# Kernel tuning notes

Hardware: AMD Instinct MI355X
Metric: run time of the kernel (lower is better)

Reference implementation:

```python
import jax, jax.numpy as jnp
import numpy as np

B, HH, WW, C, HEADS = 2, 128, 128, 256, 8
D = C // HEADS


def setup_inputs() -> dict:
    key = jax.random.key(0)
    ks = jax.random.split(key, 24)
    def nrm(k, shape, s=0.02):
        return jax.random.normal(k, shape, jnp.float32) * s
    inp = {
        'x_2': jax.random.normal(ks[0], (B, HH, WW, C), jnp.float32),
        'x_4': jax.random.normal(ks[1], (B, HH, WW, C), jnp.float32),
        'x_8': jax.random.normal(ks[2], (B, HH, WW, C), jnp.float32),
        'y':   jax.random.normal(ks[3], (B, HH, WW, C), jnp.float32),
        'Wqm': nrm(ks[4], (C, C)), 'Wkm': nrm(ks[5], (C, C)), 'Wvm': nrm(ks[6], (C, C)),
        'Wk2': nrm(ks[7], (C, C)), 'Wv2': nrm(ks[8], (C, C)),
        'Wk4': nrm(ks[9], (C, C)), 'Wv4': nrm(ks[10], (C, C)),
        'Wk8': nrm(ks[11], (C, C)), 'Wv8': nrm(ks[12], (C, C)),
        'rescalem': jnp.ones((HEADS, 1, 1), jnp.float32),
        'rescale2': jnp.ones((HEADS, 1, 1), jnp.float32),
        'rescale4': jnp.ones((HEADS, 1, 1), jnp.float32),
        'rescale8': jnp.ones((HEADS, 1, 1), jnp.float32),
        'Wproj': nrm(ks[13], (C, C)), 'bproj': jnp.zeros((C,), jnp.float32),
        'Wpos1': nrm(ks[14], (C, 1, 3, 3)), 'Wpos2': nrm(ks[15], (C, 1, 3, 3)),
    }
    return inp


def _l2norm(x):
    # F.normalize(p=2, dim=-1): x / max(||x||_2, eps)
    return x / jnp.maximum(jnp.linalg.norm(x, axis=-1, keepdims=True), 1e-12)


def _heads_T(t):
    # (b, n, h*d) -> (b, h, d, n)  (split heads then transpose last two dims)
    b, n, _ = t.shape
    return t.reshape(b, n, HEADS, D).transpose(0, 2, 3, 1)


def _dwconv(x, w):
    # x: NCHW, w: (C,1,3,3) depthwise
    return jax.lax.conv_general_dilated(
        x, w, (1, 1), 'SAME',
        dimension_numbers=('NCHW', 'OIHW', 'NCHW'),
        feature_group_count=C)


def reference(x_2, x_4, x_8, y,
              Wqm, Wkm, Wvm, Wk2, Wv2, Wk4, Wv4, Wk8, Wv8,
              rescalem, rescale2, rescale4, rescale8,
              Wproj, bproj, Wpos1, Wpos2):
    b, h, w, c = y.shape
    n = h * w
    x2 = x_2.reshape(b, n, c)
    x4 = x_4.reshape(b, n, c)
    x8 = x_8.reshape(b, n, c)
    yf = y.reshape(b, n, c)

    q_inpm = yf @ Wqm.T
    v_inpm = yf @ Wvm.T
    qm = _l2norm(_heads_T(q_inpm))  # (b,heads,d,n), L2-normalized over n

    def branch(k_inp, v_inp, rescale):
        k = _l2norm(_heads_T(k_inp))   # (b,heads,d,n)
        v = _heads_T(v_inp)            # (b,heads,d,n)
        attn = jnp.einsum('bhdn,bhen->bhde', k, qm) * rescale  # (b,heads,d,d)
        attn = jax.nn.softmax(attn, axis=-1)
        return jnp.einsum('bhde,bhen->bhdn', attn, v)

    # NOTE: original code uses rescale4 for the x8 branch (faithful to source).
    xo = (branch(yf @ Wkm.T, v_inpm, rescalem)
          + branch(x2 @ Wk2.T, x2 @ Wv2.T, rescale2)
          + branch(x4 @ Wk4.T, x4 @ Wv4.T, rescale4)
          + branch(x8 @ Wk8.T, x8 @ Wv8.T, rescale4))

    # (b,heads,d,n) -> (b,n,heads*d)
    xo = xo.transpose(0, 3, 1, 2).reshape(b, n, HEADS * D)
    out_c = (xo @ Wproj.T + bproj).reshape(b, h, w, c)

    p = v_inpm.reshape(b, h, w, c).transpose(0, 3, 1, 2)  # NCHW
    p = _dwconv(p, Wpos1)
    p = jax.nn.gelu(p, approximate=False)
    p = _dwconv(p, Wpos2)
    out_p = p.transpose(0, 2, 3, 1)

    return out_c + out_p
```

## Files before the change

kernel.cpp:

```cpp
#include <hip/hip_runtime.h>
#include <hip/hip_bf16.h>
#include <math.h>

typedef short bf16x8 __attribute__((ext_vector_type(8)));
typedef float f32x4 __attribute__((ext_vector_type(4)));

#define MFMA16(a,b,c) __builtin_amdgcn_mfma_f32_16x16x32_bf16(a,b,c,0,0,0)

__device__ inline short f2bf(float f){
  union{ __hip_bfloat16 h; short s; } u;
  u.h = __float2bfloat16(f);
  return u.s;
}
__device__ inline float bf2f(short s){
  uint32_t u = ((uint32_t)(uint16_t)s) << 16;
  return __builtin_bit_cast(float, u);
}
__device__ inline void store8bf(short* dst, float4 a, float4 b){
  union{ short s[8]; int4 q; } u;
  u.s[0]=f2bf(a.x); u.s[1]=f2bf(a.y); u.s[2]=f2bf(a.z); u.s[3]=f2bf(a.w);
  u.s[4]=f2bf(b.x); u.s[5]=f2bf(b.y); u.s[6]=f2bf(b.z); u.s[7]=f2bf(b.w);
  *(int4*)dst = u.q;
}

__device__ inline void gld16(const void* g, void* l){
  __builtin_amdgcn_global_load_lds(
      (const __attribute__((address_space(1))) unsigned int*)g,
      (__attribute__((address_space(3))) unsigned int*)l, 16, 0, 0);
}

#define BARC() do{ asm volatile("":::"memory"); __builtin_amdgcn_s_barrier(); \
                   asm volatile("":::"memory"); }while(0)

__global__ __launch_bounds__(256) void k_cvt(const float* __restrict__ src, short* __restrict__ dst, int n){
  int i = blockIdx.x*256 + threadIdx.x;
  if(i < n) dst[i] = f2bf(src[i]);
}

__global__ __launch_bounds__(256) void k_cvtN(const float* __restrict__ src, short* __restrict__ dst,
                                              int n, int ncpy){
  int i = blockIdx.x*256 + threadIdx.x;
  if(i >= n) return;
  float s = src[i];
  for(int c=1;c<ncpy;++c) s += src[i + (size_t)c*917504];
  dst[i] = f2bf(s);
}

__global__ __launch_bounds__(256) void k_wvt(const float* __restrict__ wm, const float* __restrict__ w2,
                                             const float* __restrict__ w4, const float* __restrict__ w8,
                                             short* __restrict__ wvT){
  int t = blockIdx.x*256 + threadIdx.x;
  int br = t >> 16; int rem = t & 65535; int a = rem >> 8, j = rem & 255;
  const float* w = (br==0)? wm : (br==1)? w2 : (br==2)? w4 : w8;
  wvT[t] = f2bf(w[j*256 + a]);
}

__global__ __launch_bounds__(256) void k_wT(const float* __restrict__ w1, const float* __restrict__ w2,
                                            float* __restrict__ wT){
  int t = blockIdx.x*256 + threadIdx.x;
  if(t >= 4608) return;
  int cv = t / 2304; int rem = t % 2304; int tap = rem >> 8; int c = rem & 255;
  const float* w = cv ? w2 : w1;
  wT[t] = w[c*9 + tap];
}

__global__ __launch_bounds__(256) void k_prep(const float* __restrict__ Wvm, const float* __restrict__ Wv2,
                                              const float* __restrict__ Wv4, const float* __restrict__ Wv8,
                                              const float* __restrict__ Wp1, const float* __restrict__ Wp2,
                                              short* __restrict__ WvmB, short* __restrict__ wvT,
                                              float* __restrict__ wT){
  int bx = blockIdx.x, t = threadIdx.x;
  if(bx < 256){
    int i = bx*256 + t;
    WvmB[i] = f2bf(Wvm[i]);
  } else if(bx < 1280){
    int i = (bx-256)*256 + t;
    int br = i >> 16; int rem = i & 65535; int a = rem >> 8, j = rem & 255;
    const float* w = (br==0)? Wvm : (br==1)? Wv2 : (br==2)? Wv4 : Wv8;
    wvT[i] = f2bf(w[j*256 + a]);
  } else {
    int i = (bx-1280)*256 + t;
    if(i < 4608){
      int cv = i / 2304; int rem = i % 2304; int tap = rem >> 8; int c = rem & 255;
      const float* w = cv ? Wp2 : Wp1;
      wT[i] = w[c*9 + tap];
    }
  }
}

__device__ inline void at_write4(short* base, int row, int l, float4 v){
  union{ short s[4]; int2 q; } u;
  u.s[0]=f2bf(v.x); u.s[1]=f2bf(v.y); u.s[2]=f2bf(v.z); u.s[3]=f2bf(v.w);
  int byte = row*512 + 8*l;
  byte ^= ((row&7)<<4);
  *(int2*)((char*)base + byte) = u.q;
}
__device__ inline void at_write4c(short* base, int row, int c4, float4 v){
  union{ short s[4]; int2 q; } u;
  u.s[0]=f2bf(v.x); u.s[1]=f2bf(v.y); u.s[2]=f2bf(v.z); u.s[3]=f2bf(v.w);
  int byte = row*512 + c4*8;
  byte ^= ((row&7)<<4);
  *(int2*)((char*)base + byte) = u.q;
}
__device__ inline bf16x8 at_read8(const short* base, int row, int kk, int q){
  int byte = row*512 + kk*64 + q*16;
  byte ^= ((row&7)<<4);
  return *(const bf16x8*)((const char*)base + byte);
}

__global__ __launch_bounds__(256) void k_pack(const float* __restrict__ x2, const float* __restrict__ x4,
                                              const float* __restrict__ x8, const float* __restrict__ y,
                                              short* __restrict__ xt, int sb0){
  int sb = blockIdx.z + sb0; int s = sb >> 1, b = sb & 1;
  const float* src = ((s==0)? y : (s==1)? x2 : (s==2)? x4 : x8) + (size_t)b*16384*256;
  __shared__ int4 tile4[2048];
  char* tile = (char*)tile4;
  int t = threadIdx.x;
  int cg = t & 63, ng = t >> 6;
  int n0 = blockIdx.x*64;
  const float* p0 = src + (size_t)(n0 + ng*8)*256 + cg*4;
  const float* p1 = src + (size_t)(n0 + 32 + ng*8)*256 + cg*4;
  union{ float4 q; float f[4]; } v0[8], v1[8];
  #pragma unroll
  for(int r=0;r<8;++r) v0[r].q = *(const float4*)(p0 + (size_t)r*256);
  #pragma unroll
  for(int r=0;r<8;++r) v1[r].q = *(const float4*)(p1 + (size_t)r*256);
  #pragma unroll
  for(int i=0;i<4;++i){
    int c = cg*4 + i;
    int byte = c*64 + ((ng ^ ((c>>1)&3))<<4);
    byte ^= ((byte>>8)&7)<<4;
    union{ short s8[8]; int4 q; } u;
    #pragma unroll
    for(int r=0;r<8;++r) u.s8[r] = f2bf(v0[r].f[i]);
    *(int4*)(tile + byte) = u.q;
    #pragma unroll
    for(int r=0;r<8;++r) u.s8[r] = f2bf(v1[r].f[i]);
    *(int4*)(tile + 16384 + byte) = u.q;
  }
  __syncthreads();
  short* outb = xt + ((size_t)sb*512 + blockIdx.x*2)*8192;
  #pragma unroll
  for(int ti=0; ti<2; ++ti)
    #pragma unroll
    for(int j=0;j<4;++j){
      int addr = j*4096 + t*16;
      int sa = addr ^ (((addr>>8)&7)<<4);
      *(int4*)((char*)outb + ti*16384 + addr) = *(const int4*)(tile + ti*16384 + sa);
    }
}

__global__ __launch_bounds__(256) void k_packy(const float* __restrict__ y, const short* __restrict__ wB,
                                               short* __restrict__ xt, short* __restrict__ vm){
  int b = blockIdx.z;
  const float* src = y + (size_t)b*16384*256;
  __shared__ int4 tile4[2048];
  __shared__ short at[64*256];
  char* tile = (char*)tile4;
  int t = threadIdx.x;
  int cg = t & 63, ng = t >> 6;
  int n0 = blockIdx.x*64;
  const float* p0 = src + (size_t)(n0 + ng*8)*256 + cg*4;
  const float* p1 = src + (size_t)(n0 + 32 + ng*8)*256 + cg*4;
  union{ float4 q; float f[4]; } v0[8], v1[8];
  #pragma unroll
  for(int r=0;r<8;++r) v0[r].q = *(const float4*)(p0 + (size_t)r*256);
  #pragma unroll
  for(int r=0;r<8;++r) v1[r].q = *(const float4*)(p1 + (size_t)r*256);
  #pragma unroll
  for(int i=0;i<4;++i){
    int c = cg*4 + i;
    int byte = c*64 + ((ng ^ ((c>>1)&3))<<4);
    byte ^= ((byte>>8)&7)<<4;
    union{ short s8[8]; int4 q; } u;
    #pragma unroll
    for(int r=0;r<8;++r) u.s8[r] = f2bf(v0[r].f[i]);
    *(int4*)(tile + byte) = u.q;
    #pragma unroll
    for(int r=0;r<8;++r) u.s8[r] = f2bf(v1[r].f[i]);
    *(int4*)(tile + 16384 + byte) = u.q;
  }
  #pragma unroll
  for(int r=0;r<8;++r){
    at_write4c(at, ng*8 + r, cg, v0[r].q);
    at_write4c(at, 32 + ng*8 + r, cg, v1[r].q);
  }
  __syncthreads();
  short* outb = xt + ((size_t)b*512 + blockIdx.x*2)*8192;
  #pragma unroll
  for(int ti=0; ti<2; ++ti)
    #pragma unroll
    for(int j=0;j<4;++j){
      int addr = j*4096 + t*16;
      int sa = addr ^ (((addr>>8)&7)<<4);
      *(int4*)((char*)outb + ti*16384 + addr) = *(const int4*)(tile + ti*16384 + sa);
    }
  int l = t & 63, w = t >> 6;
  size_t m0 = (size_t)b*16384 + n0;
  f32x4 acc[4][4];
  #pragma unroll
  for(int i=0;i<4;++i)
    #pragma unroll
    for(int n2=0;n2<4;++n2) acc[i][n2] = (f32x4){0.f,0.f,0.f,0.f};
  #pragma unroll
  for(int kk=0; kk<8; ++kk){
    bf16x8 a[4];
    #pragma unroll
    for(int rt=0;rt<4;++rt) a[rt] = at_read8(at, rt*16 + (l&15), kk, l>>4);
    #pragma unroll
    for(int nt=0;nt<4;++nt){
      int bc = (w*4+nt)*16 + (l&15);
      bf16x8 bb = *(const bf16x8*)&wB[(size_t)bc*256 + kk*32 + 8*(l>>4)];
      #pragma unroll
      for(int rt=0;rt<4;++rt) acc[rt][nt] = MFMA16(a[rt], bb, acc[rt][nt]);
    }
  }
  #pragma unroll
  for(int rt=0;rt<4;++rt)
    #pragma unroll
    for(int nt=0;nt<4;++nt)
      #pragma unroll
      for(int r=0;r<4;++r){
        size_t row = m0 + rt*16 + 4*(l>>4) + r;
        int col = (w*4+nt)*16 + (l&15);
        vm[row*256 + col] = f2bf(acc[rt][nt][r]);
      }
}

__device__ inline bf16x8 tfrag(const short* base, int c, int hi){
  int byte = c*64 + ((hi ^ ((c>>1)&3))<<4);
  return *(const bf16x8*)((const char*)base + byte);
}

__global__ __launch_bounds__(512) void k_cov(const short* __restrict__ xt, float* __restrict__ covF,
                                             int plain){
  int jb = blockIdx.x;
  int ck = blockIdx.y;
  int j = jb >> 1, b = jb & 1;
  int t = threadIdx.x, l = t & 63, w = t >> 6;
  int lr = l & 15, hi = l >> 4;
  int wr = w >> 1, wc = w & 1;
  __shared__ short lds2[2][32768];
  int su = (j < 4) ? 0 : (j - 3);
  int sv = (j == 0) ? 0 : ((j < 4) ? j : (j - 3));
  int sym = (su == sv);
  const short* Ug = xt + (size_t)(su*2+b)*512*8192;
  const short* Vg = xt + (size_t)(sv*2+b)*512*8192;
  int nt0 = ck*32;

  f32x4 acc[4][8];
  #pragma unroll
  for(int i=0;i<4;++i)
    #pragma unroll
    for(int n2=0;n2<8;++n2) acc[i][n2] = (f32x4){0.f,0.f,0.f,0.f};

  #define STAGE_T_S(bufi, tt, kk) do{                                           \
    const short* Ut_ = Ug + (size_t)(nt0+(kk))*8192;                            \
    short* dst_ = &lds2[bufi][(tt)*16384];                                      \
    _Pragma("unroll")                                                           \
    for(int i_=0;i_<2;++i_){ int ch_ = w*2+i_;                                  \
      gld16(Ut_ + ch_*512 + l*8, dst_ + ch_*512); }                             \
  }while(0)
  #define STAGE_T_A(bufi, tt, kk) do{                                           \
    const short* Ut_ = Ug + (size_t)(nt0+(kk))*8192;                            \
    const short* Vt_ = Vg + (size_t)(nt0+(kk))*8192;                            \
    short* dst_ = &lds2[bufi][(tt)*16384];                                      \
    _Pragma("unroll")                                                           \
    for(int i_=0;i_<4;++i_){ int ch_ = w*4+i_;                                  \
      const short* g_ = (ch_<16) ? (Ut_ + ch_*512 + l*8)                        \
                                 : (Vt_ + (ch_-16)*512 + l*8);                  \
      gld16(g_, dst_ + ch_*512); }                                              \
  }while(0)
  #define COMPUTE_T(bufp, vofs) do{                                             \
    const short* Ub_ = bufp;                                                    \
    const short* Vb_ = Ub_ + (vofs);                                            \
    bf16x8 a_[4];                                                               \
    _Pragma("unroll")                                                           \
    for(int rt_=0;rt_<4;++rt_)                                                  \
      a_[rt_] = tfrag(Ub_, wr*64 + rt_*16 + lr, hi);                            \
    _Pragma("unroll")                                                           \
    for(int nt_=0;nt_<8;++nt_){                                                 \
      bf16x8 bb_ = tfrag(Vb_, wc*128 + nt_*16 + lr, hi);                        \
      _Pragma("unroll")                                                         \
      for(int rt_=0;rt_<4;++rt_)                                                \
        acc[rt_][nt_] = MFMA16(a_[rt_], bb_, acc[rt_][nt_]);                    \
    }                                                                           \
  }while(0)

  if(sym){
    STAGE_T_S(0,0,0); STAGE_T_S(0,1,1); STAGE_T_S(1,0,2); STAGE_T_S(1,1,3);
    asm volatile("s_waitcnt vmcnt(4)":::"memory");
    BARC();
    #pragma unroll 1
    for(int p=0;p<16;++p){
      const short* base = &lds2[p&1][0];
      COMPUTE_T(base, 0);
      COMPUTE_T(base + 16384, 0);
      if(p==15) break;
      BARC();
      if(p < 14){
        STAGE_T_S(p&1, 0, 2*p+4); STAGE_T_S(p&1, 1, 2*p+5);
        asm volatile("s_waitcnt vmcnt(4)":::"memory");
      } else {
        asm volatile("s_waitcnt vmcnt(0)":::"memory");
      }
      BARC();
    }
  } else {
    STAGE_T_A(0,0,0); STAGE_T_A(0,1,1); STAGE_T_A(1,0,2); STAGE_T_A(1,1,3);
    asm volatile("s_waitcnt vmcnt(8)":::"memory");
    BARC();
    #pragma unroll 1
    for(int p=0;p<16;++p){
      const short* base = &lds2[p&1][0];
      COMPUTE_T(base, 8192);
      COMPUTE_T(base + 16384, 8192);
      if(p==15) break;
      BARC();
      if(p < 14){
        STAGE_T_A(p&1, 0, 2*p+4); STAGE_T_A(p&1, 1, 2*p+5);
        asm volatile("s_waitcnt vmcnt(8)":::"memory");
      } else {
        asm volatile("s_waitcnt vmcnt(0)":::"memory");
      }
      BARC();
    }
  }
  #undef STAGE_T_S
  #undef STAGE_T_A
  #undef COMPUTE_T

  if(plain){
    float* cov = covF + (size_t)ck*917504 + (size_t)jb*65536;
    #pragma unroll
    for(int rt=0;rt<4;++rt)
      #pragma unroll
      for(int nt=0;nt<8;++nt)
        #pragma unroll
        for(int r=0;r<4;++r){
          int row = wr*64 + rt*16 + 4*hi + r;
          int col = wc*128 + nt*16 + lr;
          cov[(size_t)row*256 + col] = acc[rt][nt][r];
        }
  } else {
    float* cov = covF + (size_t)jb*65536;
    #pragma unroll
    for(int rt=0;rt<4;++rt)
      #pragma unroll
      for(int nt=0;nt<8;++nt)
        #pragma unroll
        for(int r=0;r<4;++r){
          int row = wr*64 + rt*16 + 4*hi + r;
          int col = wc*128 + nt*16 + lr;
          atomicAdd(&cov[(size_t)row*256 + col], acc[rt][nt][r]);
        }
  }
}

__device__ inline void mm_32x256(const short (*wA)[264], const short* __restrict__ covbf,
                                 short (*tmp)[264], int t){
  int l = t & 63, w = t >> 6;
  int mt = w >> 1, ntb = (w & 1)*8;
  f32x4 acc[8];
  #pragma unroll
  for(int i=0;i<8;++i) acc[i] = (f32x4){0.f,0.f,0.f,0.f};
  #pragma unroll
  for(int kk=0; kk<8; ++kk){
    bf16x8 a = *(const bf16x8*)&wA[16*mt + (l&15)][kk*32 + 8*(l>>4)];
    #pragma unroll
    for(int n=0; n<8; ++n){
      int j = (ntb+n)*16 + (l&15);
      bf16x8 bb = *(const bf16x8*)&covbf[(size_t)j*256 + kk*32 + 8*(l>>4)];
      acc[n] = MFMA16(a, bb, acc[n]);
    }
  }
  #pragma unroll
  for(int n=0;n<8;++n)
    #pragma unroll
    for(int r=0;r<4;++r)
      tmp[16*mt + 4*(l>>4) + r][(ntb+n)*16 + (l&15)] = f2bf(acc[n][r]);
}
__device__ inline void mm_32x32(const short (*A)[264], const short (*Bw)[264], float (*M)[33], int t){
  int l = t & 63, w = t >> 6;
  int mt = w >> 1, nt = w & 1;
  f32x4 acc = (f32x4){0.f,0.f,0.f,0.f};
  #pragma unroll
  for(int kk=0; kk<8; ++kk){
    bf16x8 a = *(const bf16x8*)&A[16*mt + (l&15)][kk*32 + 8*(l>>4)];
    bf16x8 b = *(const bf16x8*)&Bw[16*nt + (l&15)][kk*32 + 8*(l>>4)];
    acc = MFMA16(a, b, acc);
  }
  #pragma unroll
  for(int r=0;r<4;++r)
    M[16*mt + 4*(l>>4) + r][16*nt + (l&15)] = acc[r];
}

__global__ __launch_bounds__(256) void k_attn(
    const float* __restrict__ Wq, const float* __restrict__ Wkm, const float* __restrict__ Wk2,
    const float* __restrict__ Wk4, const float* __restrict__ Wk8,
    const float* __restrict__ rsm, const float* __restrict__ rs2, const float* __restrict__ rs4,
    const short* __restrict__ covB, float* __restrict__ Aout){
  int h = blockIdx.x, b = blockIdx.y, br = blockIdx.z;
  int t = threadIdx.x;
  __shared__ short wk[32][264], wq[32][264], tmp[32][264];
  __shared__ float Ml[32][33];
  __shared__ float nrm[64];
  const float* Wk = (br==0)? Wkm : (br==1)? Wk2 : (br==2)? Wk4 : Wk8;
  {
    int d = t >> 3, c0 = (t & 7)*32;
    const float* pk = Wk + (size_t)(h*32+d)*256 + c0;
    const float* pq = Wq + (size_t)(h*32+d)*256 + c0;
    #pragma unroll
    for(int i=0;i<32;i+=8){
      float4 a1 = *(const float4*)(pk+i), a2 = *(const float4*)(pk+i+4);
      store8bf(&wk[d][c0+i], a1, a2);
      float4 b1 = *(const float4*)(pq+i), b2 = *(const float4*)(pq+i+4);
      store8bf(&wq[d][c0+i], b1, b2);
    }
  }
  __syncthreads();
  const short* cxy = covB + (size_t)(br*2+b)*65536;
  const short* cxx = (br==0)? cxy : covB + (size_t)(8 + (br-1)*2 + b)*65536;
  const short* cyy = covB + (size_t)b*65536;
  mm_32x256(wk, cxx, tmp, t); __syncthreads();
  mm_32x32(tmp, wk, Ml, t);   __syncthreads();
  if(t < 32) nrm[t] = Ml[t][t];
  __syncthreads();
  mm_32x256(wq, cyy, tmp, t); __syncthreads();
  mm_32x32(tmp, wq, Ml, t);   __syncthreads();
  if(t < 32) nrm[32+t] = Ml[t][t];
  __syncthreads();
  mm_32x256(wk, cxy, tmp, t); __syncthreads();
  mm_32x32(tmp, wq, Ml, t);   __syncthreads();
  if(t < 32){
    int d = t;
    const float* rs = (br==0)? rsm : (br==1)? rs2 : rs4;
    float rsv = rs[h];
    float invk = 1.f / fmaxf(sqrtf(fmaxf(nrm[d], 0.f)), 1e-12f);
    float lg[32]; float mx = -1e30f;
    #pragma unroll
    for(int e=0;e<32;++e){
      float invq = 1.f / fmaxf(sqrtf(fmaxf(nrm[32+e], 0.f)), 1e-12f);
      float v = Ml[d][e] * invk * invq * rsv;
      lg[e] = v; mx = fmaxf(mx, v);
    }
    float sum = 0.f;
    #pragma unroll
    for(int e=0;e<32;++e){ lg[e] = expf(lg[e]-mx); sum += lg[e]; }
    float inv = 1.f/sum;
    float* Ao = Aout + ((size_t)((br*2+b)*8 + h))*1024 + d*32;
    #pragma unroll
    for(int e=0;e<32;++e) Ao[e] = lg[e]*inv;
  }
}

__global__ __launch_bounds__(256) void k_qfold(const float* __restrict__ Wproj, const float* __restrict__ Ain,
                                               const short* __restrict__ wvT, short* __restrict__ qf){
  int cg = blockIdx.x, b = blockIdx.y, br = blockIdx.z;
  int t = threadIdx.x;
  __shared__ float Al[8*1036];
  __shared__ short pl[32][264];
  const float* Ag = Ain + (size_t)((br*2+b)*8)*1024;
  for(int i=t; i<8192; i+=256){
    int hh = i >> 10, dd = (i >> 5) & 31, ee = i & 31;
    Al[hh*1036 + dd*32 + ee] = Ag[i];
  }
  __syncthreads();
  {
    int c = cg*32 + (t >> 3), h = t & 7;
    const float* wpr = Wproj + (size_t)c*256 + h*32;
    float wp[32];
    #pragma unroll
    for(int i=0;i<32;i+=4){
      float4 v = *(const float4*)(wpr+i);
      wp[i]=v.x; wp[i+1]=v.y; wp[i+2]=v.z; wp[i+3]=v.w;
    }
    float pv[32];
    #pragma unroll
    for(int e=0;e<32;++e) pv[e]=0.f;
    const float* Ah = Al + h*1036;
    #pragma unroll
    for(int d=0; d<32; ++d){
      float wpd = wp[d];
      #pragma unroll
      for(int e=0;e<32;e+=4){
        float4 av = *(const float4*)&Ah[d*32+e];
        pv[e]   += wpd*av.x; pv[e+1] += wpd*av.y;
        pv[e+2] += wpd*av.z; pv[e+3] += wpd*av.w;
      }
    }
    #pragma unroll
    for(int e=0;e<32;++e) pl[t>>3][h*32+e] = f2bf(pv[e]);
  }
  __syncthreads();
  {
    int l = t & 63, w = t >> 6, mt = w >> 1, ntb = (w & 1)*8;
    const short* wvt = wvT + (size_t)br*65536;
    f32x4 acc[8];
    #pragma unroll
    for(int i=0;i<8;++i) acc[i] = (f32x4){0.f,0.f,0.f,0.f};
    #pragma unroll
    for(int kk=0; kk<8; ++kk){
      bf16x8 a = *(const bf16x8*)&pl[16*mt + (l&15)][kk*32 + 8*(l>>4)];
      #pragma unroll
      for(int n=0;n<8;++n){
        int arow = (ntb+n)*16 + (l&15);
        bf16x8 bb = *(const bf16x8*)&wvt[(size_t)arow*256 + kk*32 + 8*(l>>4)];
        acc[n] = MFMA16(a, bb, acc[n]);
      }
    }
    short* qfp = qf + (size_t)(br*2+b)*65536;
    #pragma unroll
    for(int n=0;n<8;++n)
      #pragma unroll
      for(int r=0;r<4;++r){
        int row = cg*32 + 16*mt + 4*(l>>4) + r;
        int col = (ntb+n)*16 + (l&15);
        qfp[(size_t)row*256 + col] = f2bf(acc[n][r]);
      }
  }
}

__global__ __launch_bounds__(256,2) void k_vm(const float* __restrict__ y, const short* __restrict__ wB,
                                              short* __restrict__ vm){
  int t = threadIdx.x, l = t & 63, w = t >> 6;
  size_t m0 = (size_t)blockIdx.x*64;
  __shared__ short at[64*256];
  #pragma unroll
  for(int rr=0; rr<16; ++rr){
    int row = w*16 + rr;
    float4 v = *(const float4*)(y + (m0+row)*256 + 4*l);
    at_write4(at, row, l, v);
  }
  __syncthreads();
  f32x4 acc[4][4];
  #pragma unroll
  for(int i=0;i<4;++i)
    #pragma unroll
    for(int n2=0;n2<4;++n2) acc[i][n2] = (f32x4){0.f,0.f,0.f,0.f};
  #pragma unroll
  for(int kk=0; kk<8; ++kk){
    bf16x8 a[4];
    #pragma unroll
    for(int rt=0;rt<4;++rt) a[rt] = at_read8(at, rt*16 + (l&15), kk, l>>4);
    #pragma unroll
    for(int nt=0;nt<4;++nt){
      int bc = (w*4+nt)*16 + (l&15);
      bf16x8 bb = *(const bf16x8*)&wB[(size_t)bc*256 + kk*32 + 8*(l>>4)];
      #pragma unroll
      for(int rt=0;rt<4;++rt) acc[rt][nt] = MFMA16(a[rt], bb, acc[rt][nt]);
    }
  }
  #pragma unroll
  for(int rt=0;rt<4;++rt)
    #pragma unroll
    for(int nt=0;nt<4;++nt)
      #pragma unroll
      for(int r=0;r<4;++r){
        size_t row = m0 + rt*16 + 4*(l>>4) + r;
        int col = (w*4+nt)*16 + (l&15);
        vm[row*256 + col] = f2bf(acc[rt][nt][r]);
      }
}

__global__ __launch_bounds__(256) void k_conv(const short* __restrict__ in, const float* __restrict__ wT,
                                              short* __restrict__ out, int do_gelu){
  int tid = blockIdx.x*256 + threadIdx.x;
  int cg = tid & 31; int pix = tid >> 5;
  int x = pix & 127, yy = (pix >> 7) & 127, b = pix >> 14;
  int c0 = cg*8;
  float acc[8];
  #pragma unroll
  for(int i=0;i<8;++i) acc[i]=0.f;
  #pragma unroll
  for(int ky=0; ky<3; ++ky){
    int sy = yy + ky - 1;
    if(sy < 0 || sy > 127) continue;
    #pragma unroll
    for(int kx=0; kx<3; ++kx){
      int sx = x + kx - 1;
      if(sx < 0 || sx > 127) continue;
      const float* wp = wT + (ky*3+kx)*256 + c0;
      float4 w0 = *(const float4*)wp;
      float4 w1 = *(const float4*)(wp+4);
      const short* p = in + ((size_t)(((b<<7)+sy)<<7) + sx)*256 + c0;
      union{ int4 q; short s[8]; } u;
      u.q = *(const int4*)p;
      acc[0] += bf2f(u.s[0])*w0.x; acc[1] += bf2f(u.s[1])*w0.y;
      acc[2] += bf2f(u.s[2])*w0.z; acc[3] += bf2f(u.s[3])*w0.w;
      acc[4] += bf2f(u.s[4])*w1.x; acc[5] += bf2f(u.s[5])*w1.y;
      acc[6] += bf2f(u.s[6])*w1.z; acc[7] += bf2f(u.s[7])*w1.w;
    }
  }
  if(do_gelu){
    #pragma unroll
    for(int cc=0;cc<8;++cc)
      acc[cc] = 0.5f*acc[cc]*(1.f + erff(acc[cc]*0.70710678118654752f));
  }
  union{ int4 q; short s[8]; } o;
  #pragma unroll
  for(int cc=0;cc<8;++cc) o.s[cc] = f2bf(acc[cc]);
  *(int4*)(out + (size_t)pix*256 + c0) = o.q;
}

__global__ __launch_bounds__(256,2) void k_final(const float* __restrict__ y, const float* __restrict__ x2,
                                                 const float* __restrict__ x4, const float* __restrict__ x8,
                                                 const short* __restrict__ qf, const float* __restrict__ bproj,
                                                 const short* __restrict__ pos, float* __restrict__ out){
  int t = threadIdx.x, l = t & 63, w = t >> 6;
  size_t m0 = (size_t)blockIdx.x*64;
  int b = (int)(m0 >> 14);
  __shared__ short at2[2][64*256];
  f32x4 acc[4][4];
  #pragma unroll
  for(int i=0;i<4;++i)
    #pragma unroll
    for(int n2=0;n2<4;++n2) acc[i][n2] = (f32x4){0.f,0.f,0.f,0.f};
  const float* srcs[4] = {y, x2, x4, x8};
  float4 vreg[16];
  #pragma unroll
  for(int rr=0; rr<16; ++rr)
    vreg[rr] = *(const float4*)(srcs[0] + (m0 + w*16 + rr)*256 + 4*l);
  #pragma unroll 1
  for(int br=0; br<4; ++br){
    short* buf = &at2[br&1][0];
    #pragma unroll
    for(int rr=0; rr<16; ++rr)
      at_write4(buf, w*16 + rr, l, vreg[rr]);
    if(br < 3){
      const float* s = srcs[br+1];
      #pragma unroll
      for(int rr=0; rr<16; ++rr)
        vreg[rr] = *(const float4*)(s + (m0 + w*16 + rr)*256 + 4*l);
    }
    asm volatile("s_waitcnt lgkmcnt(0)":::"memory");
    BARC();
    const short* qb = qf + (size_t)(br*2+b)*65536;
    #pragma unroll
    for(int kk=0; kk<8; ++kk){
      bf16x8 a[4];
      #pragma unroll
      for(int rt=0;rt<4;++rt) a[rt] = at_read8(buf, rt*16 + (l&15), kk, l>>4);
      #pragma unroll
      for(int nt=0;nt<4;++nt){
        int bc = (w*4+nt)*16 + (l&15);
        bf16x8 bb = *(const bf16x8*)&qb[(size_t)bc*256 + kk*32 + 8*(l>>4)];
        #pragma unroll
        for(int rt=0;rt<4;++rt) acc[rt][nt] = MFMA16(a[rt], bb, acc[rt][nt]);
      }
    }
  }
  #pragma unroll
  for(int rt=0;rt<4;++rt)
    #pragma unroll
    for(int nt=0;nt<4;++nt)
      #pragma unroll
      for(int r=0;r<4;++r){
        size_t row = m0 + rt*16 + 4*(l>>4) + r;
        int col = (w*4+nt)*16 + (l&15);
        out[row*256 + col] = acc[rt][nt][r] + bproj[col] + bf2f(pos[row*256 + col]);
      }
}

extern "C" void kernel_launch(void* const* d_in, const int* in_sizes, int n_in,
                              void* d_out, int out_size, void* d_ws, size_t ws_size,
                              hipStream_t stream){
  (void)in_sizes; (void)n_in; (void)out_size;
  const float* x2   = (const float*)d_in[0];
  const float* x4   = (const float*)d_in[1];
  const float* x8   = (const float*)d_in[2];
  const float* y    = (const float*)d_in[3];
  const float* Wq   = (const float*)d_in[4];
  const float* Wkm  = (const float*)d_in[5];
  const float* Wvm  = (const float*)d_in[6];
  const float* Wk2  = (const float*)d_in[7];
  const float* Wv2  = (const float*)d_in[8];
  const float* Wk4  = (const float*)d_in[9];
  const float* Wv4  = (const float*)d_in[10];
  const float* Wk8  = (const float*)d_in[11];
  const float* Wv8  = (const float*)d_in[12];
  const float* rsm  = (const float*)d_in[13];
  const float* rs2  = (const float*)d_in[14];
  const float* rs4  = (const float*)d_in[15];
  const float* Wproj= (const float*)d_in[17];
  const float* bproj= (const float*)d_in[18];
  const float* Wp1  = (const float*)d_in[19];
  const float* Wp2  = (const float*)d_in[20];
  float* out = (float*)d_out;

  char* ws = (char*)d_ws;
  short* XT2  = (short*)(ws + 0);
  short* GBUF = (short*)(ws + 16777216);
  short* POS  = (short*)(ws + 33554432);

  const size_t NEEDF = 146425856;
  int plain = (ws_size >= NEEDF) ? 1 : 0;

  float* covF; short* covB; float* Aout; short* QF; short* WvmB; short* WvT; float* wT; short* VM;
  if(plain){
    covF = (float*)(ws + 67108864);
    covB = (short*)(ws + 125829120);
    Aout = (float*)(ws + 127664128);
    QF   = (short*)(ws + 127926272);
    WvmB = (short*)(ws + 128974848);
    WvT  = (short*)(ws + 129105920);
    wT   = (float*)(ws + 129630208);
    VM   = (short*)(ws + 129648640);
  } else {
    covF = (float*)(ws + 67108864);
    covB = (short*)(ws + 70778880);
    Aout = (float*)(ws + 72613888);
    QF   = (short*)(ws + 72876032);
    WvmB = (short*)(ws + 73924608);
    WvT  = (short*)(ws + 74055680);
    wT   = (float*)(ws + 50331648);
    VM   = (short*)(ws + 0);
  }

  if(!plain) hipMemsetAsync(covF, 0, 3670016, stream);
  if(plain){
    k_prep<<<1298, 256, 0, stream>>>(Wvm, Wv2, Wv4, Wv8, Wp1, Wp2, WvmB, WvT, wT);
    k_packy<<<dim3(256,1,2), 256, 0, stream>>>(y, WvmB, XT2, VM);
    k_pack <<<dim3(256,1,6), 256, 0, stream>>>(x2, x4, x8, y, XT2, 2);
  } else {
    k_cvt<<<256, 256, 0, stream>>>(Wvm, WvmB, 65536);
    k_wvt<<<1024, 256, 0, stream>>>(Wvm, Wv2, Wv4, Wv8, WvT);
    k_pack<<<dim3(256,1,8), 256, 0, stream>>>(x2, x4, x8, y, XT2, 0);
  }
  k_cov  <<<dim3(14,16), 512, 0, stream>>>(XT2, covF, plain);
  k_cvtN <<<3584, 256, 0, stream>>>(covF, covB, 917504, plain ? 16 : 1);
  if(!plain) k_wT<<<18, 256, 0, stream>>>(Wp1, Wp2, wT);
  k_attn <<<dim3(8,2,4), 256, 0, stream>>>(Wq, Wkm, Wk2, Wk4, Wk8, rsm, rs2, rs4, covB, Aout);
  k_qfold<<<dim3(8,2,4), 256, 0, stream>>>(Wproj, Aout, WvT, QF);
  if(!plain) k_vm<<<512, 256, 0, stream>>>(y, WvmB, VM);
  k_conv <<<4096, 256, 0, stream>>>(VM, wT, GBUF, 1);
  k_conv <<<4096, 256, 0, stream>>>(GBUF, wT + 2304, POS, 0);
  k_final<<<512, 256, 0, stream>>>(y, x2, x4, x8, QF, bproj, POS, out);
}
```

Measured before the change: 241.0 us.

## Fuse two depthwise convs with GELU into one tiled kernel using shared-memory halo

```diff
diff --git a/kernel.cpp b/kernel.cpp
--- a/kernel.cpp
+++ b/kernel.cpp
@@ -563,44 +563,84 @@
       }
 }
 
-__global__ __launch_bounds__(256) void k_conv(const short* __restrict__ in, const float* __restrict__ wT,
-                                              short* __restrict__ out, int do_gelu){
-  int tid = blockIdx.x*256 + threadIdx.x;
-  int cg = tid & 31; int pix = tid >> 5;
-  int x = pix & 127, yy = (pix >> 7) & 127, b = pix >> 14;
-  int c0 = cg*8;
+__global__ __launch_bounds__(512) void k_convf(const short* __restrict__ vmIn,
+                                               const float* __restrict__ wT,
+                                               short* __restrict__ pos){
+  int b = blockIdx.z;
+  int x0 = blockIdx.x*4, y0 = blockIdx.y*4;
+  int t = threadIdx.x;
+  __shared__ short g1[36*256];
+  const float* w1 = wT;
+  const float* w2 = wT + 2304;
+  #pragma unroll 1
+  for(int i=0;i<3;++i){
+    int tau = t + i*512;
+    if(tau < 1152){
+      int cg1 = tau & 31, p = tau >> 5;
+      int gy = p / 6, gx = p % 6;
+      int ix = x0 - 1 + gx, iy = y0 - 1 + gy;
+      int c0 = cg1*8;
+      float acc[8];
+      #pragma unroll
+      for(int q=0;q<8;++q) acc[q]=0.f;
+      if(ix >= 0 && ix < 128 && iy >= 0 && iy < 128){
+        #pragma unroll
+        for(int ky=0; ky<3; ++ky){
+          int sy = iy + ky - 1;
+          if(sy < 0 || sy > 127) continue;
+          #pragma unroll
+          for(int kx=0; kx<3; ++kx){
+            int sx = ix + kx - 1;
+            if(sx < 0 || sx > 127) continue;
+            const float* wp = w1 + (ky*3+kx)*256 + c0;
+            float4 a0 = *(const float4*)wp;
+            float4 a1 = *(const float4*)(wp+4);
+            const short* pv = vmIn + ((size_t)(((b<<7)+sy)<<7) + sx)*256 + c0;
+            union{ int4 q; short s[8]; } u;
+            u.q = *(const int4*)pv;
+            acc[0]+=bf2f(u.s[0])*a0.x; acc[1]+=bf2f(u.s[1])*a0.y;
+            acc[2]+=bf2f(u.s[2])*a0.z; acc[3]+=bf2f(u.s[3])*a0.w;
+            acc[4]+=bf2f(u.s[4])*a1.x; acc[5]+=bf2f(u.s[5])*a1.y;
+            acc[6]+=bf2f(u.s[6])*a1.z; acc[7]+=bf2f(u.s[7])*a1.w;
+          }
+        }
+        #pragma unroll
+        for(int q=0;q<8;++q)
+          acc[q] = 0.5f*acc[q]*(1.f + erff(acc[q]*0.70710678118654752f));
+      }
+      union{ int4 q; short s[8]; } o;
+      #pragma unroll
+      for(int q=0;q<8;++q) o.s[q] = f2bf(acc[q]);
+      *(int4*)&g1[p*256 + c0] = o.q;
+    }
+  }
+  __syncthreads();
+  int cg2 = t & 31, pidx = t >> 5;
+  int px = pidx & 3, py = pidx >> 2;
+  int c0 = cg2*8;
   float acc[8];
   #pragma unroll
-  for(int i=0;i<8;++i) acc[i]=0.f;
+  for(int q=0;q<8;++q) acc[q]=0.f;
   #pragma unroll
   for(int ky=0; ky<3; ++ky){
-    int sy = yy + ky - 1;
-    if(sy < 0 || sy > 127) continue;
     #pragma unroll
     for(int kx=0; kx<3; ++kx){
-      int sx = x + kx - 1;
-      if(sx < 0 || sx > 127) continue;
-      const float* wp = wT + (ky*3+kx)*256 + c0;
-      float4 w0 = *(const float4*)wp;
-      float4 w1 = *(const float4*)(wp+4);
-      const short* p = in + ((size_t)(((b<<7)+sy)<<7) + sx)*256 + c0;
+      const float* wp = w2 + (ky*3+kx)*256 + c0;
+      float4 a0 = *(const float4*)wp;
+      float4 a1 = *(const float4*)(wp+4);
+      int gp = (py+ky)*6 + (px+kx);
       union{ int4 q; short s[8]; } u;
-      u.q = *(const int4*)p;
-      acc[0] += bf2f(u.s[0])*w0.x; acc[1] += bf2f(u.s[1])*w0.y;
-      acc[2] += bf2f(u.s[2])*w0.z; acc[3] += bf2f(u.s[3])*w0.w;
-      acc[4] += bf2f(u.s[4])*w1.x; acc[5] += bf2f(u.s[5])*w1.y;
-      acc[6] += bf2f(u.s[6])*w1.z; acc[7] += bf2f(u.s[7])*w1.w;
-    }
-  }
-  if(do_gelu){
-    #pragma unroll
-    for(int cc=0;cc<8;++cc)
-      acc[cc] = 0.5f*acc[cc]*(1.f + erff(acc[cc]*0.70710678118654752f));
+      u.q = *(const int4*)&g1[gp*256 + c0];
+      acc[0]+=bf2f(u.s[0])*a0.x; acc[1]+=bf2f(u.s[1])*a0.y;
+      acc[2]+=bf2f(u.s[2])*a0.z; acc[3]+=bf2f(u.s[3])*a0.w;
+      acc[4]+=bf2f(u.s[4])*a1.x; acc[5]+=bf2f(u.s[5])*a1.y;
+      acc[6]+=bf2f(u.s[6])*a1.z; acc[7]+=bf2f(u.s[7])*a1.w;
+    }
   }
   union{ int4 q; short s[8]; } o;
   #pragma unroll
-  for(int cc=0;cc<8;++cc) o.s[cc] = f2bf(acc[cc]);
-  *(int4*)(out + (size_t)pix*256 + c0) = o.q;
+  for(int q=0;q<8;++q) o.s[q] = f2bf(acc[q]);
+  *(int4*)(pos + ((size_t)(((b<<7)+(y0+py))<<7) + (x0+px))*256 + c0) = o.q;
 }
 
 __global__ __launch_bounds__(256,2) void k_final(const float* __restrict__ y, const float* __restrict__ x2,
@@ -690,7 +730,6 @@
 
   char* ws = (char*)d_ws;
   short* XT2  = (short*)(ws + 0);
-  short* GBUF = (short*)(ws + 16777216);
   short* POS  = (short*)(ws + 33554432);
 
   const size_t NEEDF = 146425856;
@@ -733,7 +772,6 @@
   k_attn <<<dim3(8,2,4), 256, 0, stream>>>(Wq, Wkm, Wk2, Wk4, Wk8, rsm, rs2, rs4, covB, Aout);
   k_qfold<<<dim3(8,2,4), 256, 0, stream>>>(Wproj, Aout, WvT, QF);
   if(!plain) k_vm<<<512, 256, 0, stream>>>(y, WvmB, VM);
-  k_conv <<<4096, 256, 0, stream>>>(VM, wT, GBUF, 1);
-  k_conv <<<4096, 256, 0, stream>>>(GBUF, wT + 2304, POS, 0);
+  k_convf<<<dim3(32,32,2), 512, 0, stream>>>(VM, wT, POS);
   k_final<<<512, 256, 0, stream>>>(y, x2, x4, x8, QF, bproj, POS, out);
 }
```

Result: slower. 247.6 us (+2.7%).
